# Optimization experiments

Measured on AMD Instinct MI355X. Metric: run time of the kernel, lower is better.

The kernel has to match this reference:

```python
import jax, jax.numpy as jnp
import numpy as np

N, E = 50000, 800000
INDIM, HID, OUT = 128, 256, 47
DENSITY = 0.5
EPS = 1e-5


def _masked_glorot(key, fan_in, fan_out):
    kw, km = jax.random.split(key)
    lim = np.sqrt(6.0 / (fan_in + fan_out))
    w = jax.random.uniform(kw, (fan_in, fan_out), jnp.float32, -lim, lim)
    mask = (jax.random.uniform(km, (fan_in, fan_out)) < DENSITY).astype(jnp.float32)
    return w * mask  # expander sparsity pre-applied to the weight


def setup_inputs() -> dict:
    key = jax.random.key(0)
    ks = jax.random.split(key, 12)
    x = jax.random.normal(ks[0], (N, INDIM), jnp.float32)
    edge_index = jax.random.randint(ks[1], (2, E), 0, N, jnp.int64)
    d = {
        "x": x,
        "edge_index": edge_index,
        "w1l": _masked_glorot(ks[2], INDIM, HID),
        "w1r": _masked_glorot(ks[3], INDIM, HID),
        "b1": jnp.zeros((HID,), jnp.float32),
        "g1": jnp.ones((HID,), jnp.float32),
        "be1": jnp.zeros((HID,), jnp.float32),
        "w2l": _masked_glorot(ks[4], HID, HID),
        "w2r": _masked_glorot(ks[5], HID, HID),
        "b2": jnp.zeros((HID,), jnp.float32),
        "g2": jnp.ones((HID,), jnp.float32),
        "be2": jnp.zeros((HID,), jnp.float32),
        "w3l": _masked_glorot(ks[6], HID, OUT),
        "w3r": _masked_glorot(ks[7], HID, OUT),
        "b3": jnp.zeros((OUT,), jnp.float32),
    }
    return d


def reference(x, edge_index, w1l, w1r, b1, g1, be1, w2l, w2r, b2, g2, be2, w3l, w3r, b3):
    src, dst = edge_index[0], edge_index[1]
    n = x.shape[0]
    deg = jax.ops.segment_sum(jnp.ones(src.shape[0], x.dtype), dst, num_segments=n)
    inv_deg = 1.0 / jnp.maximum(deg, 1.0)  # [N]

    def sage(h, wl, wr, b):
        # mean-aggregate neighbor features (gather + segment_sum), then masked linears
        agg = jax.ops.segment_sum(h[src], dst, num_segments=n) * inv_deg[:, None]
        return agg @ wl + h @ wr + b

    def bn(h, g, b):
        mu = h.mean(axis=0)
        var = h.var(axis=0)
        return g * (h - mu) * jax.lax.rsqrt(var + EPS) + b

    h = jax.nn.relu(bn(sage(x, w1l, w1r, b1), g1, be1))
    h = jax.nn.relu(bn(sage(h, w2l, w2r, b2), g2, be2))
    h = sage(h, w3l, w3r, b3)
    return jax.nn.log_softmax(h, axis=-1)
```

## Files before the change

### kernel.cpp

```cpp
#include <hip/hip_runtime.h>
#include <hip/hip_bf16.h>
#include <cmath>

#define EPS 1e-5f

typedef __attribute__((ext_vector_type(8))) short bf16x8;
typedef __attribute__((ext_vector_type(4))) float f32x4;
typedef __attribute__((ext_vector_type(2))) float floatx2;

static __device__ __forceinline__ ushort f32_to_bf16(float f) {
    __hip_bfloat16 h = __float2bfloat16(f);
    return __builtin_bit_cast(ushort, h);
}
static __device__ __forceinline__ float blo(unsigned u) { return __uint_as_float(u << 16); }
static __device__ __forceinline__ float bhi(unsigned u) { return __uint_as_float(u & 0xffff0000u); }
static __device__ __forceinline__ unsigned bpack(float a, float b) {
    return (unsigned)f32_to_bf16(a) | ((unsigned)f32_to_bf16(b) << 16);
}
static __device__ __forceinline__ unsigned char f32_to_fp8(float v) {
    return (unsigned char)(__builtin_amdgcn_cvt_pk_fp8_f32(v, 0.f, 0, false) & 0xff);
}

static __device__ __forceinline__ void async16(const void* g, void* l) {
    __builtin_amdgcn_global_load_lds(
        (const __attribute__((address_space(1))) unsigned int*)g,
        (__attribute__((address_space(3))) unsigned int*)l, 16, 0, 0);
}

#define DEC8(u) { floatx2 p_; \
    p_ = __builtin_amdgcn_cvt_pk_f32_fp8((int)(u).x, false); a0 += p_.x; a1 += p_.y; \
    p_ = __builtin_amdgcn_cvt_pk_f32_fp8((int)(u).x, true);  a2 += p_.x; a3 += p_.y; \
    p_ = __builtin_amdgcn_cvt_pk_f32_fp8((int)(u).y, false); a4 += p_.x; a5 += p_.y; \
    p_ = __builtin_amdgcn_cvt_pk_f32_fp8((int)(u).y, true);  a6 += p_.x; a7 += p_.y; }
#define DEC4(u) { floatx2 p_; \
    p_ = __builtin_amdgcn_cvt_pk_f32_fp8((int)(u), false); a0 += p_.x; a1 += p_.y; \
    p_ = __builtin_amdgcn_cvt_pk_f32_fp8((int)(u), true);  a2 += p_.x; a3 += p_.y; }


__global__ void k_pre(const int* __restrict__ dst, int E, int* __restrict__ gcnt,
                      const float* __restrict__ x, ushort* __restrict__ cat1,
                      unsigned char* __restrict__ xq, int NX,
                      const float* __restrict__ w1l, const float* __restrict__ w1r,
                      const float* __restrict__ w2l, const float* __restrict__ w2r,
                      const float* __restrict__ w3l, const float* __restrict__ w3r,
                      ushort* __restrict__ Wt1, ushort* __restrict__ Wt2,
                      ushort* __restrict__ Wt3, int bktB, int cvtB) {
    int b = blockIdx.x;
    int t = threadIdx.x;
    if (b < bktB) {
        __shared__ int hist[256];
        hist[t] = 0;
        __syncthreads();
        int base = b * 8192;
        int end = base + 8192; if (end > E) end = E;
        for (int i = base + t; i < end; i += 256)
            atomicAdd(&hist[((unsigned)dst[i]) >> 8], 1);
        __syncthreads();
        if (hist[t]) atomicAdd(&gcnt[t], hist[t]);
    } else if (b < bktB + cvtB) {
        int i = (b - bktB) * 256 + t;
        if (i < NX) {
            int row = i >> 7, c = i & 127;
            float v = x[i];
            cat1[(size_t)row * 256 + 128 + c] = f32_to_bf16(v);
            xq[(size_t)row * 128 + c] = f32_to_fp8(v);
        }
    } else {
        int tt = (b - bktB - cvtB) * 256 + t;
        if (tt < 128 * 256) {
            int k = tt >> 8, c = tt & 255;
            Wt1[(size_t)c * 256 + k] = f32_to_bf16(w1l[tt]);
            Wt1[(size_t)c * 256 + 128 + k] = f32_to_bf16(w1r[tt]);
        }
        if (tt < 256 * 256) {
            int k = tt >> 8, c = tt & 255;
            Wt2[(size_t)c * 512 + k] = f32_to_bf16(w2l[tt]);
            Wt2[(size_t)c * 512 + 256 + k] = f32_to_bf16(w2r[tt]);
        }
        if (tt < 256 * 47) {
            int k = tt / 47, c = tt - k * 47;
            Wt3[(size_t)c * 256 + k] = f32_to_bf16(w3l[tt]);
            Wt3[(size_t)(64 + c) * 256 + k] = f32_to_bf16(w3r[tt]);
        }
    }
}

__global__ void k_bscan(const int* __restrict__ gcnt, int* __restrict__ gbase,
                        int* __restrict__ gtail, int NB) {
    __shared__ int s[256];
    int t = threadIdx.x;
    int v = (t < NB) ? gcnt[t] : 0;
    s[t] = v;
    __syncthreads();
    for (int off = 1; off < 256; off <<= 1) {
        int add = (t >= off) ? s[t - off] : 0;
        __syncthreads();
        s[t] += add;
        __syncthreads();
    }
    int excl = s[t] - v;
    if (t < NB) { gbase[t] = excl; gtail[t] = excl; }
}

__global__ void k_scatter(const int* __restrict__ src, const int* __restrict__ dst,
                          int E, int* __restrict__ gtail, uint2* __restrict__ pairs,
                          int NB) {
    __shared__ int hist[256];
    __shared__ int lcur[256];
    int t = threadIdx.x;
    hist[t] = 0;
    __syncthreads();
    int base = blockIdx.x * 8192;
    int end = base + 8192; if (end > E) end = E;
    for (int i = base + t; i < end; i += 256)
        atomicAdd(&hist[((unsigned)dst[i]) >> 8], 1);
    __syncthreads();
    if (t < NB && hist[t]) lcur[t] = atomicAdd(&gtail[t], hist[t]);
    __syncthreads();
    for (int i = base + t; i < end; i += 256) {
        int dd = dst[i];
        int pos = atomicAdd(&lcur[((unsigned)dd) >> 8], 1);
        pairs[pos] = make_uint2((unsigned)src[i], (unsigned)dd);
    }
}

__global__ void k_brow(const uint2* __restrict__ pairs, const int* __restrict__ gbase,
                       const int* __restrict__ gcnt, int* __restrict__ row_ptr,
                       float* __restrict__ inv_deg, int N, int E) {
    int b = blockIdx.x;
    __shared__ int hist[256];
    __shared__ int sc[256];
    int t = threadIdx.x;
    hist[t] = 0;
    __syncthreads();
    int s = gbase[b], cnt = gcnt[b];
    for (int i = t; i < cnt; i += 256) {
        uint2 p = pairs[s + i];
        atomicAdd(&hist[p.y & 255], 1);
    }
    __syncthreads();
    int d = hist[t];
    sc[t] = d;
    __syncthreads();
    for (int off = 1; off < 256; off <<= 1) {
        int add = (t >= off) ? sc[t - off] : 0;
        __syncthreads();
        sc[t] += add;
        __syncthreads();
    }
    int node = b * 256 + t;
    if (node < N) {
        row_ptr[node] = s + sc[t] - d;
        inv_deg[node] = 1.0f / (float)(d > 1 ? d : 1);
    }
    if (b == 0 && t == 0) row_ptr[N] = E;
}

__global__ void k_bfill(const uint2* __restrict__ pairs, const int* __restrict__ gbase,
                        const int* __restrict__ gcnt, const int* __restrict__ row_ptr,
                        int* __restrict__ colidx, int N) {
    int b = blockIdx.x;
    __shared__ int cur[256];
    int t = threadIdx.x;
    int node = b * 256 + t;
    cur[t] = (node < N) ? row_ptr[node] : 0;
    __syncthreads();
    int s = gbase[b], cnt = gcnt[b];
    for (int i = t; i < cnt; i += 256) {
        uint2 p = pairs[s + i];
        int pos = atomicAdd(&cur[p.y & 255], 1);
        colidx[pos] = (int)p.x;
    }
}


__global__ void k_agg256q(const unsigned char* __restrict__ hq, const int* __restrict__ rp,
                          const int* __restrict__ ci, const float* __restrict__ inv_deg,
                          ushort* __restrict__ out, int ldo, int N) {
    int wid = (blockIdx.x * blockDim.x + threadIdx.x) >> 6;
    int lane = threadIdx.x & 63;
    if (wid >= N) return;
    int s = rp[wid], e = rp[wid + 1];
    int half = lane >> 5, l32 = lane & 31;
    int cnt = e - s;
    int n_my = (cnt - half + 1) >> 1;
    int i = s + half;
    float a0 = 0, a1 = 0, a2 = 0, a3 = 0, a4 = 0, a5 = 0, a6 = 0, a7 = 0;
    size_t lo = (size_t)l32 * 8;
    while (n_my >= 4) {
        int c0 = ci[i], c1 = ci[i + 2], c2 = ci[i + 4], c3 = ci[i + 6];
        uint2 u0 = *reinterpret_cast<const uint2*>(hq + (size_t)c0 * 256 + lo);
        uint2 u1 = *reinterpret_cast<const uint2*>(hq + (size_t)c1 * 256 + lo);
        uint2 u2 = *reinterpret_cast<const uint2*>(hq + (size_t)c2 * 256 + lo);
        uint2 u3 = *reinterpret_cast<const uint2*>(hq + (size_t)c3 * 256 + lo);
        DEC8(u0); DEC8(u1); DEC8(u2); DEC8(u3);
        i += 8; n_my -= 4;
    }
    while (n_my > 0) {
        int c = ci[i];
        uint2 u = *reinterpret_cast<const uint2*>(hq + (size_t)c * 256 + lo);
        DEC8(u);
        i += 2; n_my--;
    }
    a0 += __shfl_xor(a0, 32, 64); a1 += __shfl_xor(a1, 32, 64);
    a2 += __shfl_xor(a2, 32, 64); a3 += __shfl_xor(a3, 32, 64);
    a4 += __shfl_xor(a4, 32, 64); a5 += __shfl_xor(a5, 32, 64);
    a6 += __shfl_xor(a6, 32, 64); a7 += __shfl_xor(a7, 32, 64);
    if (half == 0) {
        float id = inv_deg[wid];
        uint4 o;
        o.x = bpack(a0 * id, a1 * id); o.y = bpack(a2 * id, a3 * id);
        o.z = bpack(a4 * id, a5 * id); o.w = bpack(a6 * id, a7 * id);
        *reinterpret_cast<uint4*>(out + (size_t)wid * ldo + l32 * 8) = o;
    }
}

__global__ void k_agg128q(const unsigned char* __restrict__ hq, const int* __restrict__ rp,
                          const int* __restrict__ ci, const float* __restrict__ inv_deg,
                          ushort* __restrict__ out, int ldo, int N) {
    int wid = (blockIdx.x * blockDim.x + threadIdx.x) >> 6;
    int lane = threadIdx.x & 63;
    if (wid >= N) return;
    int s = rp[wid], e = rp[wid + 1];
    int g = lane >> 4, l16 = lane & 15;
    int cnt = e - s;
    int n_my = (cnt - g + 3) >> 2;
    int i = s + g;
    float a0 = 0, a1 = 0, a2 = 0, a3 = 0, a4 = 0, a5 = 0, a6 = 0, a7 = 0;
    size_t lo = (size_t)l16 * 8;
    while (n_my >= 4) {
        int c0 = ci[i], c1 = ci[i + 4], c2 = ci[i + 8], c3 = ci[i + 12];
        uint2 u0 = *reinterpret_cast<const uint2*>(hq + (size_t)c0 * 128 + lo);
        uint2 u1 = *reinterpret_cast<const uint2*>(hq + (size_t)c1 * 128 + lo);
        uint2 u2 = *reinterpret_cast<const uint2*>(hq + (size_t)c2 * 128 + lo);
        uint2 u3 = *reinterpret_cast<const uint2*>(hq + (size_t)c3 * 128 + lo);
        DEC8(u0); DEC8(u1); DEC8(u2); DEC8(u3);
        i += 16; n_my -= 4;
    }
    while (n_my > 0) {
        int c = ci[i];
        uint2 u = *reinterpret_cast<const uint2*>(hq + (size_t)c * 128 + lo);
        DEC8(u);
        i += 4; n_my--;
    }
#pragma unroll
    for (int off = 16; off <= 32; off <<= 1) {
        a0 += __shfl_xor(a0, off, 64); a1 += __shfl_xor(a1, off, 64);
        a2 += __shfl_xor(a2, off, 64); a3 += __shfl_xor(a3, off, 64);
        a4 += __shfl_xor(a4, off, 64); a5 += __shfl_xor(a5, off, 64);
        a6 += __shfl_xor(a6, off, 64); a7 += __shfl_xor(a7, off, 64);
    }
    if (lane < 16) {
        float id = inv_deg[wid];
        uint4 o;
        o.x = bpack(a0 * id, a1 * id); o.y = bpack(a2 * id, a3 * id);
        o.z = bpack(a4 * id, a5 * id); o.w = bpack(a6 * id, a7 * id);
        *reinterpret_cast<uint4*>(out + (size_t)wid * ldo + l16 * 8) = o;
    }
}

__global__ void k_agg47fq(const unsigned char* __restrict__ p3q, const int* __restrict__ rp,
                          const int* __restrict__ ci, const float* __restrict__ inv_deg,
                          const float* __restrict__ q3, float* __restrict__ out,
                          int N, int OUTD) {
    int wid = (blockIdx.x * blockDim.x + threadIdx.x) >> 6;
    int lane = threadIdx.x & 63;
    if (wid >= N) return;
    int s = rp[wid], e = rp[wid + 1];
    int g = lane >> 4, l16 = lane & 15;
    int cnt = e - s;
    int n_my = (cnt - g + 3) >> 2;
    int i = s + g;
    float a0 = 0, a1 = 0, a2 = 0, a3 = 0;
    size_t lo = (size_t)l16 * 4;
    while (n_my >= 4) {
        int c0 = ci[i], c1 = ci[i + 4], c2 = ci[i + 8], c3 = ci[i + 12];
        unsigned u0 = *reinterpret_cast<const unsigned*>(p3q + (size_t)c0 * 64 + lo);
        unsigned u1 = *reinterpret_cast<const unsigned*>(p3q + (size_t)c1 * 64 + lo);
        unsigned u2 = *reinterpret_cast<const unsigned*>(p3q + (size_t)c2 * 64 + lo);
        unsigned u3 = *reinterpret_cast<const unsigned*>(p3q + (size_t)c3 * 64 + lo);
        DEC4(u0); DEC4(u1); DEC4(u2); DEC4(u3);
        i += 16; n_my -= 4;
    }
    while (n_my > 0) {
        int c = ci[i];
        unsigned u = *reinterpret_cast<const unsigned*>(p3q + (size_t)c * 64 + lo);
        DEC4(u);
        i += 4; n_my--;
    }
#pragma unroll
    for (int off = 16; off <= 32; off <<= 1) {
        a0 += __shfl_xor(a0, off, 64); a1 += __shfl_xor(a1, off, 64);
        a2 += __shfl_xor(a2, off, 64); a3 += __shfl_xor(a3, off, 64);
    }
    float id = inv_deg[wid];
    int c0 = l16 * 4;
    float z0 = (c0 + 0 < OUTD) ? a0 * id + q3[(size_t)wid * 48 + c0 + 0] : -INFINITY;
    float z1 = (c0 + 1 < OUTD) ? a1 * id + q3[(size_t)wid * 48 + c0 + 1] : -INFINITY;
    float z2 = (c0 + 2 < OUTD) ? a2 * id + q3[(size_t)wid * 48 + c0 + 2] : -INFINITY;
    float z3 = (c0 + 3 < OUTD) ? a3 * id + q3[(size_t)wid * 48 + c0 + 3] : -INFINITY;
    float m = fmaxf(fmaxf(z0, z1), fmaxf(z2, z3));
#pragma unroll
    for (int off = 1; off <= 8; off <<= 1) m = fmaxf(m, __shfl_xor(m, off, 64));
    float es = ((c0 + 0 < OUTD) ? __expf(z0 - m) : 0.f) + ((c0 + 1 < OUTD) ? __expf(z1 - m) : 0.f)
             + ((c0 + 2 < OUTD) ? __expf(z2 - m) : 0.f) + ((c0 + 3 < OUTD) ? __expf(z3 - m) : 0.f);
#pragma unroll
    for (int off = 1; off <= 8; off <<= 1) es += __shfl_xor(es, off, 64);
    float ls = __logf(es) + m;
    if (lane < 16) {
        if (c0 + 0 < OUTD) out[(size_t)wid * OUTD + c0 + 0] = z0 - ls;
        if (c0 + 1 < OUTD) out[(size_t)wid * OUTD + c0 + 1] = z1 - ls;
        if (c0 + 2 < OUTD) out[(size_t)wid * OUTD + c0 + 2] = z2 - ls;
        if (c0 + 3 < OUTD) out[(size_t)wid * OUTD + c0 + 3] = z3 - ls;
    }
}


template <int EPI>
__global__ __launch_bounds__(256) void k_mgemm(
    const ushort* __restrict__ A, const ushort* __restrict__ Wt,
    const float* __restrict__ bias, ushort* __restrict__ outb,
    unsigned char* __restrict__ outq,
    float* __restrict__ q3, float* __restrict__ psum, float* __restrict__ psq,
    int Nrows, int K, int M) {
    __shared__ __align__(16) ushort sA[64 * 32];
    __shared__ __align__(16) ushort sB[128 * 32];
    __shared__ float red[2][2][4][16][2];
    const int tid = threadIdx.x;
    const int w = tid >> 6, l = tid & 63;
    const int wr = w >> 1, wc = w & 1;
    const int row0 = blockIdx.x * 64, col0 = blockIdx.y * 128;
    const int li = l & 15, kg = l >> 4;

    f32x4 acc[2][4] = {};

    for (int kt = 0; kt < K; kt += 32) {
        {
            int c = tid;
            int r = c >> 2, kgp = c & 3;
            int kgl = (kgp - (r >> 1)) & 3;
            int gr = row0 + r;
            if (gr >= Nrows) gr = Nrows - 1;
            async16(A + (size_t)gr * K + kt + kgl * 8, &sA[(size_t)c * 8]);
        }
#pragma unroll
        for (int i = 0; i < 2; i++) {
            int c = tid + i * 256;
            int r = c >> 2, kgp = c & 3;
            int kgl = (kgp - (r >> 1)) & 3;
            async16(Wt + (size_t)(col0 + r) * K + kt + kgl * 8, &sB[(size_t)c * 8]);
        }
        __syncthreads();

        bf16x8 af[2], bfr[4];
#pragma unroll
        for (int m = 0; m < 2; m++) {
            int r = wr * 32 + m * 16 + li;
            af[m] = *reinterpret_cast<const bf16x8*>(&sA[(r * 4 + ((kg + (r >> 1)) & 3)) * 8]);
        }
#pragma unroll
        for (int n = 0; n < 4; n++) {
            int r = wc * 64 + n * 16 + li;
            bfr[n] = *reinterpret_cast<const bf16x8*>(&sB[(r * 4 + ((kg + (r >> 1)) & 3)) * 8]);
        }
#pragma unroll
        for (int m = 0; m < 2; m++)
#pragma unroll
            for (int n = 0; n < 4; n++)
                acc[m][n] = __builtin_amdgcn_mfma_f32_16x16x32_bf16(af[m], bfr[n], acc[m][n], 0, 0, 0);
        __syncthreads();
    }

    if constexpr (EPI == 2) {
#pragma unroll
        for (int n = 0; n < 4; n++) {
            int col = col0 + wc * 64 + n * 16 + li;
            float b = bias[col];
            float s = 0.f, sq = 0.f;
#pragma unroll
            for (int m = 0; m < 2; m++) {
                int rbase = row0 + wr * 32 + m * 16 + kg * 4;
#pragma unroll
                for (int qi = 0; qi < 4; qi++) {
                    int row = rbase + qi;
                    if (row < Nrows) {
                        float v = acc[m][n][qi] + b;
                        outb[(size_t)row * M + col] = f32_to_bf16(v);
                        s += v; sq += v * v;
                    }
                }
            }
            s += __shfl_xor(s, 16, 64); s += __shfl_xor(s, 32, 64);
            sq += __shfl_xor(sq, 16, 64); sq += __shfl_xor(sq, 32, 64);
            if (kg == 0) { red[wr][wc][n][li][0] = s; red[wr][wc][n][li][1] = sq; }
        }
        __syncthreads();
        if (wr == 0 && kg == 0) {
#pragma unroll
            for (int n = 0; n < 4; n++) {
                int gcol = col0 + wc * 64 + n * 16 + li;
                psum[(size_t)gcol * 1024 + blockIdx.x] = red[0][wc][n][li][0] + red[1][wc][n][li][0];
                psq[(size_t)gcol * 1024 + blockIdx.x] = red[0][wc][n][li][1] + red[1][wc][n][li][1];
            }
        }
    } else {
#pragma unroll
        for (int n = 0; n < 4; n++) {
            int col = wc * 64 + n * 16 + li;
#pragma unroll
            for (int m = 0; m < 2; m++) {
                int rbase = row0 + wr * 32 + m * 16 + kg * 4;
#pragma unroll
                for (int qi = 0; qi < 4; qi++) {
                    int row = rbase + qi;
                    if (row >= Nrows) continue;
                    float v = acc[m][n][qi];
                    if (wc == 0) {
                        outq[(size_t)row * 64 + col] = f32_to_fp8(col < 47 ? v : 0.f);
                    } else {
                        int qc = col - 64;
                        if (qc < 47) q3[(size_t)row * 48 + qc] = v + bias[qc];
                    }
                }
            }
        }
    }
}


__global__ void k_bn_final(const float* __restrict__ psum, const float* __restrict__ psq,
                           int nb, int N, const float* __restrict__ g,
                           const float* __restrict__ be, float* __restrict__ scale,
                           float* __restrict__ shift) {
    int c = blockIdx.x;
    int t = threadIdx.x;
    float s = 0.f, q = 0.f;
    for (int b = t; b < nb; b += 256) { s += psum[(size_t)c * 1024 + b]; q += psq[(size_t)c * 1024 + b]; }
#pragma unroll
    for (int off = 32; off; off >>= 1) { s += __shfl_xor(s, off, 64); q += __shfl_xor(q, off, 64); }
    __shared__ float ls[4], lq[4];
    int wv = t >> 6;
    if ((t & 63) == 0) { ls[wv] = s; lq[wv] = q; }
    __syncthreads();
    if (t == 0) {
        s = ls[0] + ls[1] + ls[2] + ls[3];
        q = lq[0] + lq[1] + lq[2] + lq[3];
        float mu = s / (float)N;
        float var = q / (float)N - mu * mu;
        float sc = g[c] * rsqrtf(var + EPS);
        scale[c] = sc;
        shift[c] = be[c] - mu * sc;
    }
}

__global__ void k_bn_apply_b(const ushort* __restrict__ zb, long total8,
                             const float* __restrict__ scale, const float* __restrict__ shift,
                             ushort* __restrict__ outb, int ldo, int off,
                             unsigned char* __restrict__ hq) {
    long i = blockIdx.x * (long)blockDim.x + threadIdx.x;
    long stride = (long)gridDim.x * blockDim.x;
    for (; i < total8; i += stride) {
        long idx = i * 8;
        int row = (int)(idx >> 8);
        int c = (int)(idx & 255);
        uint4 u = *reinterpret_cast<const uint4*>(zb + idx);
        float y0 = fmaxf(blo(u.x) * scale[c + 0] + shift[c + 0], 0.f);
        float y1 = fmaxf(bhi(u.x) * scale[c + 1] + shift[c + 1], 0.f);
        float y2 = fmaxf(blo(u.y) * scale[c + 2] + shift[c + 2], 0.f);
        float y3 = fmaxf(bhi(u.y) * scale[c + 3] + shift[c + 3], 0.f);
        float y4 = fmaxf(blo(u.z) * scale[c + 4] + shift[c + 4], 0.f);
        float y5 = fmaxf(bhi(u.z) * scale[c + 5] + shift[c + 5], 0.f);
        float y6 = fmaxf(blo(u.w) * scale[c + 6] + shift[c + 6], 0.f);
        float y7 = fmaxf(bhi(u.w) * scale[c + 7] + shift[c + 7], 0.f);
        uint4 o;
        o.x = bpack(y0, y1); o.y = bpack(y2, y3); o.z = bpack(y4, y5); o.w = bpack(y6, y7);
        *reinterpret_cast<uint4*>(outb + (size_t)row * ldo + off + c) = o;
        if (hq) {
            unsigned lo8 = 0, hi8 = 0;
            lo8 = (unsigned)__builtin_amdgcn_cvt_pk_fp8_f32(y0, y1, 0, false);
            lo8 = (unsigned)__builtin_amdgcn_cvt_pk_fp8_f32(y2, y3, (int)lo8, true);
            hi8 = (unsigned)__builtin_amdgcn_cvt_pk_fp8_f32(y4, y5, 0, false);
            hi8 = (unsigned)__builtin_amdgcn_cvt_pk_fp8_f32(y6, y7, (int)hi8, true);
            *reinterpret_cast<uint2*>(hq + (size_t)row * 256 + c) = make_uint2(lo8, hi8);
        }
    }
}


extern "C" void kernel_launch(void* const* d_in, const int* in_sizes, int n_in,
                              void* d_out, int out_size, void* d_ws, size_t ws_size,
                              hipStream_t stream) {
    const float* x   = (const float*)d_in[0];
    const int*   ei  = (const int*)d_in[1];
    const float* w1l = (const float*)d_in[2];
    const float* w1r = (const float*)d_in[3];
    const float* b1  = (const float*)d_in[4];
    const float* g1  = (const float*)d_in[5];
    const float* be1 = (const float*)d_in[6];
    const float* w2l = (const float*)d_in[7];
    const float* w2r = (const float*)d_in[8];
    const float* b2  = (const float*)d_in[9];
    const float* g2  = (const float*)d_in[10];
    const float* be2 = (const float*)d_in[11];
    const float* w3l = (const float*)d_in[12];
    const float* w3r = (const float*)d_in[13];
    const float* b3  = (const float*)d_in[14];
    float* out = (float*)d_out;

    const int INDIM = 128, HID = 256;
    int N = in_sizes[0] / INDIM;
    int E = in_sizes[1] / 2;
    int OUTD = in_sizes[14];
    const int* src = ei;
    const int* dst = ei + E;
    int NB = (N + 255) >> 8;

    size_t off = 0;
    auto carve = [&](size_t bytes) -> char* {
        char* p = (char*)d_ws + off;
        off = (off + bytes + 255) & ~(size_t)255;
        return p;
    };
    int*    row_ptr  = (int*)carve((size_t)(N + 1) * 4);
    float*  inv_deg  = (float*)carve((size_t)N * 4);
    int*    gcnt     = (int*)carve(256 * 4);
    int*    gbase    = (int*)carve(256 * 4);
    int*    gtail    = (int*)carve(256 * 4);
    uint2*  pairs    = (uint2*)carve((size_t)E * 8);
    int*    colidx   = (int*)carve((size_t)E * 4);
    float*  psum     = (float*)carve((size_t)256 * 1024 * 4);
    float*  psq      = (float*)carve((size_t)256 * 1024 * 4);
    float*  bnscale  = (float*)carve(256 * 4);
    float*  bnshift  = (float*)carve(256 * 4);
    ushort* Wt1      = (ushort*)carve((size_t)256 * 256 * 2);
    ushort* Wt2      = (ushort*)carve((size_t)256 * 512 * 2);
    ushort* Wt3      = (ushort*)carve((size_t)128 * 256 * 2);
    ushort* cat1     = (ushort*)carve((size_t)N * 256 * 2);
    unsigned char* xq  = (unsigned char*)carve((size_t)N * 128);
    unsigned char* h1q = (unsigned char*)carve((size_t)N * 256);
    ushort* cat2     = (ushort*)carve((size_t)N * 512 * 2);
    ushort* zb       = (ushort*)carve((size_t)N * HID * 2);
    unsigned char* p3q = (unsigned char*)carve((size_t)N * 64);
    float*  q3       = (float*)carve((size_t)N * 48 * 4);
    (void)ws_size; (void)n_in; (void)out_size;

    hipMemsetAsync(gcnt, 0, 256 * 4, stream);
    hipMemsetAsync(Wt3, 0, (size_t)128 * 256 * 2, stream);

    int bktB = (E + 8191) / 8192;
    int cvtB = (N * 128 + 255) / 256;
    k_pre<<<bktB + cvtB + 256, 256, 0, stream>>>(dst, E, gcnt, x, cat1, xq, N * 128,
                                                 w1l, w1r, w2l, w2r, w3l, w3r,
                                                 Wt1, Wt2, Wt3, bktB, cvtB);
    k_bscan<<<1, 256, 0, stream>>>(gcnt, gbase, gtail, NB);
    k_scatter<<<bktB, 256, 0, stream>>>(src, dst, E, gtail, pairs, NB);
    k_brow<<<NB, 256, 0, stream>>>(pairs, gbase, gcnt, row_ptr, inv_deg, N, E);
    k_bfill<<<NB, 256, 0, stream>>>(pairs, gbase, gcnt, row_ptr, colidx, N);

    int aggBlocks = (N + 3) / 4;
    int MB = (N + 63) / 64;
    long total8 = (long)N * 32;
    ushort* h2b = cat2;

    k_agg128q<<<aggBlocks, 256, 0, stream>>>(xq, row_ptr, colidx, inv_deg, cat1, 256, N);
    k_mgemm<2><<<dim3(MB, 2), 256, 0, stream>>>(cat1, Wt1, b1, zb, nullptr, nullptr,
                                                psum, psq, N, 256, 256);
    k_bn_final<<<256, 256, 0, stream>>>(psum, psq, MB, N, g1, be1, bnscale, bnshift);
    k_bn_apply_b<<<1024, 256, 0, stream>>>(zb, total8, bnscale, bnshift, cat2, 512, 256, h1q);

    k_agg256q<<<aggBlocks, 256, 0, stream>>>(h1q, row_ptr, colidx, inv_deg, cat2, 512, N);
    k_mgemm<2><<<dim3(MB, 2), 256, 0, stream>>>(cat2, Wt2, b2, zb, nullptr, nullptr,
                                                psum, psq, N, 512, 256);
    k_bn_final<<<256, 256, 0, stream>>>(psum, psq, MB, N, g2, be2, bnscale, bnshift);
    k_bn_apply_b<<<1024, 256, 0, stream>>>(zb, total8, bnscale, bnshift, h2b, 256, 0, nullptr);

    k_mgemm<1><<<dim3(MB, 1), 256, 0, stream>>>(h2b, Wt3, b3, nullptr, p3q, q3,
                                                nullptr, nullptr, N, 256, 128);
    k_agg47fq<<<aggBlocks, 256, 0, stream>>>(p3q, row_ptr, colidx, inv_deg, q3, out, N, OUTD);
}
```

Baseline: 282.0 us.

## Double-buffer GEMM LDS tiles and transpose BN partial-sum layout

```diff
diff --git a/kernel.cpp b/kernel.cpp
--- a/kernel.cpp
+++ b/kernel.cpp
@@ -323,8 +323,8 @@
     unsigned char* __restrict__ outq,
     float* __restrict__ q3, float* __restrict__ psum, float* __restrict__ psq,
     int Nrows, int K, int M) {
-    __shared__ __align__(16) ushort sA[64 * 32];
-    __shared__ __align__(16) ushort sB[128 * 32];
+    __shared__ __align__(16) ushort sA[2][64 * 32];
+    __shared__ __align__(16) ushort sB[2][128 * 32];
     __shared__ float red[2][2][4][16][2];
     const int tid = threadIdx.x;
     const int w = tid >> 6, l = tid & 63;
@@ -332,43 +332,56 @@
     const int row0 = blockIdx.x * 64, col0 = blockIdx.y * 128;
     const int li = l & 15, kg = l >> 4;
 
+    const int rA = tid >> 2, kgpA = tid & 3;
+    const int kglA = (kgpA - (rA >> 1)) & 3;
+    int grA = row0 + rA; if (grA >= Nrows) grA = Nrows - 1;
+    const ushort* gpA = A + (size_t)grA * K + kglA * 8;
+
+    const int rB0 = tid >> 2, kglB0 = ((tid & 3) - (rB0 >> 1)) & 3;
+    const ushort* gpB0 = Wt + (size_t)(col0 + rB0) * K + kglB0 * 8;
+    const int cB1 = tid + 256;
+    const int rB1 = cB1 >> 2, kglB1 = ((cB1 & 3) - (rB1 >> 1)) & 3;
+    const ushort* gpB1 = Wt + (size_t)(col0 + rB1) * K + kglB1 * 8;
+
     f32x4 acc[2][4] = {};
 
-    for (int kt = 0; kt < K; kt += 32) {
-        {
-            int c = tid;
-            int r = c >> 2, kgp = c & 3;
-            int kgl = (kgp - (r >> 1)) & 3;
-            int gr = row0 + r;
-            if (gr >= Nrows) gr = Nrows - 1;
-            async16(A + (size_t)gr * K + kt + kgl * 8, &sA[(size_t)c * 8]);
-        }
-#pragma unroll
-        for (int i = 0; i < 2; i++) {
-            int c = tid + i * 256;
-            int r = c >> 2, kgp = c & 3;
-            int kgl = (kgp - (r >> 1)) & 3;
-            async16(Wt + (size_t)(col0 + r) * K + kt + kgl * 8, &sB[(size_t)c * 8]);
-        }
-        __syncthreads();
+    const int nk = K >> 5;
+    async16(gpA, &sA[0][(size_t)tid * 8]);
+    async16(gpB0, &sB[0][(size_t)tid * 8]);
+    async16(gpB1, &sB[0][(size_t)cB1 * 8]);
+
+    for (int t = 0; t < nk; ++t) {
+        const int cur = t & 1;
+        if (t + 1 < nk) {
+            const int kt = (t + 1) << 5;
+            async16(gpA + kt, &sA[cur ^ 1][(size_t)tid * 8]);
+            async16(gpB0 + kt, &sB[cur ^ 1][(size_t)tid * 8]);
+            async16(gpB1 + kt, &sB[cur ^ 1][(size_t)cB1 * 8]);
+            asm volatile("s_waitcnt vmcnt(3)" ::: "memory");
+        } else {
+            asm volatile("s_waitcnt vmcnt(0)" ::: "memory");
+        }
+        __builtin_amdgcn_s_barrier();
+        __builtin_amdgcn_sched_barrier(0);
 
         bf16x8 af[2], bfr[4];
 #pragma unroll
         for (int m = 0; m < 2; m++) {
             int r = wr * 32 + m * 16 + li;
-            af[m] = *reinterpret_cast<const bf16x8*>(&sA[(r * 4 + ((kg + (r >> 1)) & 3)) * 8]);
+            af[m] = *reinterpret_cast<const bf16x8*>(&sA[cur][(r * 4 + ((kg + (r >> 1)) & 3)) * 8]);
         }
 #pragma unroll
         for (int n = 0; n < 4; n++) {
             int r = wc * 64 + n * 16 + li;
-            bfr[n] = *reinterpret_cast<const bf16x8*>(&sB[(r * 4 + ((kg + (r >> 1)) & 3)) * 8]);
+            bfr[n] = *reinterpret_cast<const bf16x8*>(&sB[cur][(r * 4 + ((kg + (r >> 1)) & 3)) * 8]);
         }
 #pragma unroll
         for (int m = 0; m < 2; m++)
 #pragma unroll
             for (int n = 0; n < 4; n++)
                 acc[m][n] = __builtin_amdgcn_mfma_f32_16x16x32_bf16(af[m], bfr[n], acc[m][n], 0, 0, 0);
-        __syncthreads();
+        __builtin_amdgcn_sched_barrier(0);
+        __builtin_amdgcn_s_barrier();
     }
 
     if constexpr (EPI == 2) {
@@ -399,8 +412,8 @@
 #pragma unroll
             for (int n = 0; n < 4; n++) {
                 int gcol = col0 + wc * 64 + n * 16 + li;
-                psum[(size_t)gcol * 1024 + blockIdx.x] = red[0][wc][n][li][0] + red[1][wc][n][li][0];
-                psq[(size_t)gcol * 1024 + blockIdx.x] = red[0][wc][n][li][1] + red[1][wc][n][li][1];
+                psum[(size_t)blockIdx.x * 256 + gcol] = red[0][wc][n][li][0] + red[1][wc][n][li][0];
+                psq[(size_t)blockIdx.x * 256 + gcol] = red[0][wc][n][li][1] + red[1][wc][n][li][1];
             }
         }
     } else {
@@ -435,7 +448,7 @@
     int c = blockIdx.x;
     int t = threadIdx.x;
     float s = 0.f, q = 0.f;
-    for (int b = t; b < nb; b += 256) { s += psum[(size_t)c * 1024 + b]; q += psq[(size_t)c * 1024 + b]; }
+    for (int b = t; b < nb; b += 256) { s += psum[(size_t)b * 256 + c]; q += psq[(size_t)b * 256 + c]; }
 #pragma unroll
     for (int off = 32; off; off >>= 1) { s += __shfl_xor(s, off, 64); q += __shfl_xor(q, off, 64); }
     __shared__ float ls[4], lq[4];
```

Result: no change. 281.8 us (-0.1%).

## Make GEMM persistent over row tiles with resident weights and async A pipeline

Applied to the files above, without the earlier changes.

```diff
diff --git a/kernel.cpp b/kernel.cpp
--- a/kernel.cpp
+++ b/kernel.cpp
@@ -316,112 +316,160 @@
 }
 
 
-template <int EPI>
-__global__ __launch_bounds__(256) void k_mgemm(
+template <int EPI, int COLS, int K>
+__global__ __launch_bounds__(256) void k_pgemm(
     const ushort* __restrict__ A, const ushort* __restrict__ Wt,
     const float* __restrict__ bias, ushort* __restrict__ outb,
-    unsigned char* __restrict__ outq,
-    float* __restrict__ q3, float* __restrict__ psum, float* __restrict__ psq,
-    int Nrows, int K, int M) {
-    __shared__ __align__(16) ushort sA[64 * 32];
-    __shared__ __align__(16) ushort sB[128 * 32];
-    __shared__ float red[2][2][4][16][2];
+    unsigned char* __restrict__ outq, float* __restrict__ q3,
+    float* __restrict__ psum, float* __restrict__ psq,
+    int Nrows, int G, int nrt) {
+    constexpr int NK = K / 32;
+    constexpr int LGNK = (NK == 16) ? 4 : 3;
+    constexpr int NACC = COLS / 32;
+    constexpr int DEPTH = 4;
+    constexpr int NBI = (COLS * K) / 2048;
+
+    __shared__ __align__(16) ushort sB[COLS * K];
+    __shared__ __align__(16) ushort sA[DEPTH][64 * 32];
+    __shared__ float red[2][2][NACC][16][2];
+
     const int tid = threadIdx.x;
     const int w = tid >> 6, l = tid & 63;
     const int wr = w >> 1, wc = w & 1;
-    const int row0 = blockIdx.x * 64, col0 = blockIdx.y * 128;
     const int li = l & 15, kg = l >> 4;
-
-    f32x4 acc[2][4] = {};
-
-    for (int kt = 0; kt < K; kt += 32) {
-        {
-            int c = tid;
-            int r = c >> 2, kgp = c & 3;
-            int kgl = (kgp - (r >> 1)) & 3;
-            int gr = row0 + r;
-            if (gr >= Nrows) gr = Nrows - 1;
-            async16(A + (size_t)gr * K + kt + kgl * 8, &sA[(size_t)c * 8]);
-        }
-#pragma unroll
-        for (int i = 0; i < 2; i++) {
-            int c = tid + i * 256;
-            int r = c >> 2, kgp = c & 3;
-            int kgl = (kgp - (r >> 1)) & 3;
-            async16(Wt + (size_t)(col0 + r) * K + kt + kgl * 8, &sB[(size_t)c * 8]);
-        }
-        __syncthreads();
-
-        bf16x8 af[2], bfr[4];
+    const int col0 = blockIdx.y * COLS;
+    const int rt0 = blockIdx.x * G;
+    int ntiles = nrt - rt0; if (ntiles > G) ntiles = G;
+    const int total = ntiles << LGNK;
+
+    const int rA = tid >> 2, kgpA = tid & 3;
+    const int kglA = (kgpA - (rA >> 1)) & 3;
+
+#pragma unroll
+    for (int i = 0; i < NBI; i++) {
+        int cc = tid + i * 256;
+        int ktb = cc / (COLS * 4);
+        int ct = cc & (COLS * 4 - 1);
+        int r = ct >> 2, kgp = ct & 3;
+        int kgl = (kgp - (r >> 1)) & 3;
+        async16(Wt + (size_t)(col0 + r) * K + ktb * 32 + kgl * 8, &sB[(size_t)cc * 8]);
+    }
+
+    auto issueA = [&](int s) {
+        int rtl = s >> LGNK;
+        int kt = s & (NK - 1);
+        int row = (rt0 + rtl) * 64 + rA;
+        if (row >= Nrows) row = Nrows - 1;
+        async16(A + (size_t)row * K + kt * 32 + kglA * 8, &sA[s & (DEPTH - 1)][(size_t)tid * 8]);
+    };
+
+#pragma unroll
+    for (int s = 0; s < DEPTH - 1; s++) issueA(s);
+
+    f32x4 acc[2][NACC];
+#pragma unroll
+    for (int m = 0; m < 2; m++)
+#pragma unroll
+        for (int n = 0; n < NACC; n++) acc[m][n] = (f32x4){0.f, 0.f, 0.f, 0.f};
+    float sacc[NACC], sqacc[NACC];
+#pragma unroll
+    for (int n = 0; n < NACC; n++) { sacc[n] = 0.f; sqacc[n] = 0.f; }
+
+    for (int s = 0; s < total; ++s) {
+        int lead = total - 1 - s; if (lead > DEPTH - 2) lead = DEPTH - 2;
+        if (lead == 2)      asm volatile("s_waitcnt vmcnt(2)" ::: "memory");
+        else if (lead == 1) asm volatile("s_waitcnt vmcnt(1)" ::: "memory");
+        else                asm volatile("s_waitcnt vmcnt(0)" ::: "memory");
+        __builtin_amdgcn_s_barrier();
+        __builtin_amdgcn_sched_barrier(0);
+
+        if (s + DEPTH - 1 < total) issueA(s + DEPTH - 1);
+
+        const int kt = s & (NK - 1);
+        const ushort* sBk = sB + (size_t)kt * (COLS * 32);
+        const int buf = s & (DEPTH - 1);
+
+        bf16x8 af[2], bfr[NACC];
 #pragma unroll
         for (int m = 0; m < 2; m++) {
             int r = wr * 32 + m * 16 + li;
-            af[m] = *reinterpret_cast<const bf16x8*>(&sA[(r * 4 + ((kg + (r >> 1)) & 3)) * 8]);
-        }
-#pragma unroll
-        for (int n = 0; n < 4; n++) {
-            int r = wc * 64 + n * 16 + li;
-            bfr[n] = *reinterpret_cast<const bf16x8*>(&sB[(r * 4 + ((kg + (r >> 1)) & 3)) * 8]);
+            af[m] = *reinterpret_cast<const bf16x8*>(&sA[buf][(r * 4 + ((kg + (r >> 1)) & 3)) * 8]);
+        }
+#pragma unroll
+        for (int n = 0; n < NACC; n++) {
+            int r = wc * (COLS / 2) + n * 16 + li;
+            bfr[n] = *reinterpret_cast<const bf16x8*>(&sBk[(r * 4 + ((kg + (r >> 1)) & 3)) * 8]);
         }
 #pragma unroll
         for (int m = 0; m < 2; m++)
 #pragma unroll
-            for (int n = 0; n < 4; n++)
+            for (int n = 0; n < NACC; n++)
                 acc[m][n] = __builtin_amdgcn_mfma_f32_16x16x32_bf16(af[m], bfr[n], acc[m][n], 0, 0, 0);
-        __syncthreads();
-    }
-
-    if constexpr (EPI == 2) {
-#pragma unroll
-        for (int n = 0; n < 4; n++) {
-            int col = col0 + wc * 64 + n * 16 + li;
-            float b = bias[col];
-            float s = 0.f, sq = 0.f;
-#pragma unroll
-            for (int m = 0; m < 2; m++) {
-                int rbase = row0 + wr * 32 + m * 16 + kg * 4;
-#pragma unroll
-                for (int qi = 0; qi < 4; qi++) {
-                    int row = rbase + qi;
-                    if (row < Nrows) {
-                        float v = acc[m][n][qi] + b;
-                        outb[(size_t)row * M + col] = f32_to_bf16(v);
-                        s += v; sq += v * v;
+
+        if (kt == NK - 1) {
+            int row0 = (rt0 + (s >> LGNK)) * 64;
+            if constexpr (EPI == 2) {
+#pragma unroll
+                for (int n = 0; n < NACC; n++) {
+                    int col = col0 + wc * (COLS / 2) + n * 16 + li;
+                    float b = bias[col];
+#pragma unroll
+                    for (int m = 0; m < 2; m++) {
+                        int rbase = row0 + wr * 32 + m * 16 + kg * 4;
+#pragma unroll
+                        for (int qi = 0; qi < 4; qi++) {
+                            int row = rbase + qi;
+                            if (row < Nrows) {
+                                float v = acc[m][n][qi] + b;
+                                outb[(size_t)row * 256 + col] = f32_to_bf16(v);
+                                sacc[n] += v; sqacc[n] += v * v;
+                            }
+                        }
+                        acc[m][n] = (f32x4){0.f, 0.f, 0.f, 0.f};
+                    }
+                }
+            } else {
+#pragma unroll
+                for (int n = 0; n < NACC; n++) {
+                    int col = wc * (COLS / 2) + n * 16 + li;
+#pragma unroll
+                    for (int m = 0; m < 2; m++) {
+                        int rbase = row0 + wr * 32 + m * 16 + kg * 4;
+#pragma unroll
+                        for (int qi = 0; qi < 4; qi++) {
+                            int row = rbase + qi;
+                            if (row < Nrows) {
+                                float v = acc[m][n][qi];
+                                if (wc == 0) {
+                                    outq[(size_t)row * 64 + col] = f32_to_fp8(col < 47 ? v : 0.f);
+                                } else {
+                                    int qc = col - 64;
+                                    if (qc < 47) q3[(size_t)row * 48 + qc] = v + bias[qc];
+                                }
+                            }
+                        }
+                        acc[m][n] = (f32x4){0.f, 0.f, 0.f, 0.f};
                     }
                 }
             }
-            s += __shfl_xor(s, 16, 64); s += __shfl_xor(s, 32, 64);
-            sq += __shfl_xor(sq, 16, 64); sq += __shfl_xor(sq, 32, 64);
-            if (kg == 0) { red[wr][wc][n][li][0] = s; red[wr][wc][n][li][1] = sq; }
+        }
+    }
+
+    if constexpr (EPI == 2) {
+#pragma unroll
+        for (int n = 0; n < NACC; n++) {
+            float s_ = sacc[n], q_ = sqacc[n];
+            s_ += __shfl_xor(s_, 16, 64); s_ += __shfl_xor(s_, 32, 64);
+            q_ += __shfl_xor(q_, 16, 64); q_ += __shfl_xor(q_, 32, 64);
+            if (kg == 0) { red[wr][wc][n][li][0] = s_; red[wr][wc][n][li][1] = q_; }
         }
         __syncthreads();
         if (wr == 0 && kg == 0) {
 #pragma unroll
-            for (int n = 0; n < 4; n++) {
-                int gcol = col0 + wc * 64 + n * 16 + li;
-                psum[(size_t)gcol * 1024 + blockIdx.x] = red[0][wc][n][li][0] + red[1][wc][n][li][0];
-                psq[(size_t)gcol * 1024 + blockIdx.x] = red[0][wc][n][li][1] + red[1][wc][n][li][1];
-            }
-        }
-    } else {
-#pragma unroll
-        for (int n = 0; n < 4; n++) {
-            int col = wc * 64 + n * 16 + li;
-#pragma unroll
-            for (int m = 0; m < 2; m++) {
-                int rbase = row0 + wr * 32 + m * 16 + kg * 4;
-#pragma unroll
-                for (int qi = 0; qi < 4; qi++) {
-                    int row = rbase + qi;
-                    if (row >= Nrows) continue;
-                    float v = acc[m][n][qi];
-                    if (wc == 0) {
-                        outq[(size_t)row * 64 + col] = f32_to_fp8(col < 47 ? v : 0.f);
-                    } else {
-                        int qc = col - 64;
-                        if (qc < 47) q3[(size_t)row * 48 + qc] = v + bias[qc];
-                    }
-                }
+            for (int n = 0; n < NACC; n++) {
+                int gcol = col0 + wc * (COLS / 2) + n * 16 + li;
+                psum[(size_t)blockIdx.x * 256 + gcol] = red[0][wc][n][li][0] + red[1][wc][n][li][0];
+                psq[(size_t)blockIdx.x * 256 + gcol]  = red[0][wc][n][li][1] + red[1][wc][n][li][1];
             }
         }
     }
@@ -435,7 +483,7 @@
     int c = blockIdx.x;
     int t = threadIdx.x;
     float s = 0.f, q = 0.f;
-    for (int b = t; b < nb; b += 256) { s += psum[(size_t)c * 1024 + b]; q += psq[(size_t)c * 1024 + b]; }
+    for (int b = t; b < nb; b += 256) { s += psum[(size_t)b * 256 + c]; q += psq[(size_t)b * 256 + c]; }
 #pragma unroll
     for (int off = 32; off; off >>= 1) { s += __shfl_xor(s, off, 64); q += __shfl_xor(q, off, 64); }
     __shared__ float ls[4], lq[4];
@@ -558,23 +606,27 @@
     k_bfill<<<NB, 256, 0, stream>>>(pairs, gbase, gcnt, row_ptr, colidx, N);
 
     int aggBlocks = (N + 3) / 4;
-    int MB = (N + 63) / 64;
+    int MBt = (N + 63) >> 6;
+    const int G1 = 3, G2 = 6, G3 = 3;
+    int gx1 = (MBt + G1 - 1) / G1;
+    int gx2 = (MBt + G2 - 1) / G2;
+    int gx3 = (MBt + G3 - 1) / G3;
     long total8 = (long)N * 32;
     ushort* h2b = cat2;
 
     k_agg128q<<<aggBlocks, 256, 0, stream>>>(xq, row_ptr, colidx, inv_deg, cat1, 256, N);
-    k_mgemm<2><<<dim3(MB, 2), 256, 0, stream>>>(cat1, Wt1, b1, zb, nullptr, nullptr,
-                                                psum, psq, N, 256, 256);
-    k_bn_final<<<256, 256, 0, stream>>>(psum, psq, MB, N, g1, be1, bnscale, bnshift);
+    k_pgemm<2, 256, 256><<<dim3(gx1, 1), 256, 0, stream>>>(cat1, Wt1, b1, zb, nullptr, nullptr,
+                                                           psum, psq, N, G1, MBt);
+    k_bn_final<<<256, 256, 0, stream>>>(psum, psq, gx1, N, g1, be1, bnscale, bnshift);
     k_bn_apply_b<<<1024, 256, 0, stream>>>(zb, total8, bnscale, bnshift, cat2, 512, 256, h1q);
 
     k_agg256q<<<aggBlocks, 256, 0, stream>>>(h1q, row_ptr, colidx, inv_deg, cat2, 512, N);
-    k_mgemm<2><<<dim3(MB, 2), 256, 0, stream>>>(cat2, Wt2, b2, zb, nullptr, nullptr,
-                                                psum, psq, N, 512, 256);
-    k_bn_final<<<256, 256, 0, stream>>>(psum, psq, MB, N, g2, be2, bnscale, bnshift);
+    k_pgemm<2, 128, 512><<<dim3(gx2, 2), 256, 0, stream>>>(cat2, Wt2, b2, zb, nullptr, nullptr,
+                                                           psum, psq, N, G2, MBt);
+    k_bn_final<<<256, 256, 0, stream>>>(psum, psq, gx2, N, g2, be2, bnscale, bnshift);
     k_bn_apply_b<<<1024, 256, 0, stream>>>(zb, total8, bnscale, bnshift, h2b, 256, 0, nullptr);
 
-    k_mgemm<1><<<dim3(MB, 1), 256, 0, stream>>>(h2b, Wt3, b3, nullptr, p3q, q3,
-                                                nullptr, nullptr, N, 256, 128);
+    k_pgemm<1, 128, 256><<<dim3(gx3, 1), 256, 0, stream>>>(h2b, Wt3, b3, nullptr, p3q, q3,
+                                                           nullptr, nullptr, N, G3, MBt);
     k_agg47fq<<<aggBlocks, 256, 0, stream>>>(p3q, row_ptr, colidx, inv_deg, q3, out, N, OUTD);
 }
```

Result: slower. 464.1 us (+64.6%).
